# Optimization experiments

Measured on AMD Instinct MI355X. Metric: run time of the kernel, lower is better.

## Reference

```python
import jax, jax.numpy as jnp
import numpy as np

B, C, E, H = 8, 2048, 1024, 128


def setup_inputs() -> dict:
    key = jax.random.key(0)
    k1, k2, k3, k4 = jax.random.split(key, 4)
    x = jax.random.normal(k1, (B, C, E), dtype=jnp.float32)
    # store projection weights as (E, H) so projection is x @ W
    Wq = jax.random.normal(k2, (E, H), dtype=jnp.float32) * (E ** -0.5)
    Wk = jax.random.normal(k3, (E, H), dtype=jnp.float32) * (E ** -0.5)
    Wv = jax.random.normal(k4, (E, H), dtype=jnp.float32) * (E ** -0.5)
    return {"x": x, "Wq": Wq, "Wk": Wk, "Wv": Wv}


def reference(x, Wq, Wk, Wv):
    # x: (B, C, E) -> out: (B, C, H)
    _, c, e = x.shape
    q = x @ Wq  # (B, C, H)
    k = x @ Wk  # (B, C, H)
    v = x @ Wv  # (B, C, H)
    # NOTE: original scales by embed_size**0.5, not head_size**0.5
    scale = jnp.asarray(e, x.dtype) ** 0.5
    w = jnp.einsum('bqh,bkh->bqk', q, k) / scale  # (B, C, C)
    causal = jnp.tril(jnp.ones((c, c), dtype=bool))
    w = jnp.where(causal, w, -jnp.inf)
    w = jax.nn.softmax(w, axis=-1)
    # dropout_rate = 0.0 -> identity (eval mode)
    out = w @ v  # (B, C, H)
    return out
```

## Files before the change

### kernel.cpp

```cpp
#include <hip/hip_runtime.h>
#include <hip/hip_bf16.h>
#include <stdint.h>

#define B_ 8
#define C_ 2048
#define E_ 1024
#define H_ 128
#define M_ (B_*C_)
#define SLOTS_B 144

typedef __attribute__((ext_vector_type(8))) short bf16x8;
typedef __attribute__((ext_vector_type(4))) float f32x4;

__device__ __forceinline__ unsigned short f2bf(float f) {
    union { float f; unsigned int u; } v; v.f = f;
    unsigned int u = v.u;
    u += 0x7fff + ((u >> 16) & 1);
    return (unsigned short)(u >> 16);
}
__device__ __forceinline__ float bf2f(unsigned short u) {
    union { unsigned int i; float f; } v; v.i = ((unsigned int)u) << 16; return v.f;
}

#define GLOAD_LDS16(g, l) \
    __builtin_amdgcn_global_load_lds((const __attribute__((address_space(1))) void*)(g), \
                                     (__attribute__((address_space(3))) void*)(l), 16, 0, 0)

__global__ __launch_bounds__(256) void wt_kernel(const float* __restrict__ Wq,
                                                 const float* __restrict__ Wk,
                                                 const float* __restrict__ Wv,
                                                 unsigned short* __restrict__ WT) {
    int z = blockIdx.y;
    const float* W = (z == 0) ? Wq : (z == 1) ? Wk : Wv;
    unsigned short* o = WT + (size_t)z * H_ * E_;
    int idx = blockIdx.x * 256 + threadIdx.x;
    int e = idx & (E_ - 1), h = idx >> 10;
    o[(size_t)h * E_ + e] = f2bf(W[(size_t)e * H_ + h]);
}

__global__ __launch_bounds__(256) void proj_kernel(const float* __restrict__ x,
                                                   const unsigned short* __restrict__ WT,
                                                   unsigned short* __restrict__ QKV) {
    __shared__ __align__(16) unsigned short As[2][64][64];
    __shared__ __align__(16) unsigned short Bs[2][128][64];

    const int tid = threadIdx.x;
    const int wid = tid >> 6, lane = tid & 63;
    const int lrow = lane & 15, lq = lane >> 4;
    const int wr = wid >> 1, wc = wid & 1;
    const int row0 = blockIdx.x * 64;
    const int w = blockIdx.y;
    const unsigned short* wt = WT + (size_t)w * H_ * E_;

    const int arow = tid >> 2;
    const int ag0 = (tid & 3) * 2;
    const float* xrow = x + (size_t)(row0 + arow) * E_ + ag0 * 8;

    f32x4 acc[2][4];
#pragma unroll
    for (int mi = 0; mi < 2; ++mi)
#pragma unroll
        for (int ni = 0; ni < 4; ++ni) acc[mi][ni] = (f32x4){0.f, 0.f, 0.f, 0.f};

    float4 a0, a1, a2, a3;
    auto A_LOAD = [&](int t) {
        const float* xs = xrow + t * 64;
        a0 = *(const float4*)xs;       a1 = *(const float4*)(xs + 4);
        a2 = *(const float4*)(xs + 8); a3 = *(const float4*)(xs + 12);
    };
    auto A_WRITE = [&](int buf) {
        unsigned short t0[8] = {f2bf(a0.x), f2bf(a0.y), f2bf(a0.z), f2bf(a0.w),
                                f2bf(a1.x), f2bf(a1.y), f2bf(a1.z), f2bf(a1.w)};
        unsigned short t1[8] = {f2bf(a2.x), f2bf(a2.y), f2bf(a2.z), f2bf(a2.w),
                                f2bf(a3.x), f2bf(a3.y), f2bf(a3.z), f2bf(a3.w)};
        *(bf16x8*)&As[buf][arow][(ag0 ^ (arow & 7)) * 8]       = *(const bf16x8*)t0;
        *(bf16x8*)&As[buf][arow][((ag0 + 1) ^ (arow & 7)) * 8] = *(const bf16x8*)t1;
    };
    auto B_STAGE = [&](int buf, int t) {
#pragma unroll
        for (int s = 0; s < 4; ++s) {
            int brow = s * 32 + (tid >> 3);
            int bg = (tid & 7) ^ (brow & 7);
            GLOAD_LDS16(wt + (size_t)brow * E_ + t * 64 + bg * 8,
                        (char*)&Bs[buf][0][0] + s * 4096 + tid * 16);
        }
    };
    auto COMPUTE = [&](int buf) {
#pragma unroll
        for (int ks = 0; ks < 2; ++ks) {
            const int g = ks * 4 + lq;
            bf16x8 af[2], bfr[4];
#pragma unroll
            for (int mi = 0; mi < 2; ++mi) {
                int ra = wr * 32 + mi * 16 + lrow;
                af[mi] = *(const bf16x8*)&As[buf][ra][(g ^ (ra & 7)) * 8];
            }
#pragma unroll
            for (int ni = 0; ni < 4; ++ni) {
                int rb = wc * 64 + ni * 16 + lrow;
                bfr[ni] = *(const bf16x8*)&Bs[buf][rb][(g ^ (rb & 7)) * 8];
            }
#pragma unroll
            for (int mi = 0; mi < 2; ++mi)
#pragma unroll
                for (int ni = 0; ni < 4; ++ni)
                    acc[mi][ni] = __builtin_amdgcn_mfma_f32_16x16x32_bf16(af[mi], bfr[ni], acc[mi][ni], 0, 0, 0);
        }
    };

    A_LOAD(0);
    B_STAGE(0, 0);
    A_WRITE(0);

    for (int t = 0; t < 16; ++t) {
        const int cur = t & 1;
        __syncthreads();
        if (t < 15) {
            A_LOAD(t + 1);
            B_STAGE(cur ^ 1, t + 1);
        }
        COMPUTE(cur);
        if (t < 15) A_WRITE(cur ^ 1);
    }

    if (w < 2) {
        const float qs = (w == 0) ? 0.03125f : 1.0f;
        unsigned short* outp = QKV + (size_t)w * M_ * H_;
#pragma unroll
        for (int mi = 0; mi < 2; ++mi) {
            int r0 = row0 + wr * 32 + mi * 16 + lq * 4;
#pragma unroll
            for (int ni = 0; ni < 4; ++ni) {
                int col = wc * 64 + ni * 16 + lrow;
#pragma unroll
                for (int r = 0; r < 4; ++r)
                    outp[(size_t)(r0 + r) * H_ + col] = f2bf(acc[mi][ni][r] * qs);
            }
        }
    } else {
        unsigned short* vt = QKV + (size_t)2 * M_ * H_;
        int b = row0 / C_;
        int cbase = row0 % C_;
#pragma unroll
        for (int mi = 0; mi < 2; ++mi) {
            int c0 = cbase + wr * 32 + mi * 16 + lq * 4;
#pragma unroll
            for (int ni = 0; ni < 4; ++ni) {
                int h = wc * 64 + ni * 16 + lrow;
                __align__(8) unsigned short p[4] = {f2bf(acc[mi][ni][0]), f2bf(acc[mi][ni][1]),
                                                    f2bf(acc[mi][ni][2]), f2bf(acc[mi][ni][3])};
                *(uint2*)&vt[((size_t)b * H_ + h) * C_ + c0] = *(const uint2*)p;
            }
        }
    }
}

__global__ __launch_bounds__(256) void attn_kernel(const unsigned short* __restrict__ QKV,
                                                   unsigned short* __restrict__ PO,
                                                   float* __restrict__ ML,
                                                   float* __restrict__ out) {
    __shared__ __align__(16) unsigned short Ks[2][64][128];
    __shared__ __align__(16) unsigned short Vt[2][128][64];
    __shared__ __align__(16) unsigned short Ps[4][16][72];

    const unsigned short* Q  = QKV;
    const unsigned short* K  = QKV + (size_t)M_ * H_;
    const unsigned short* VT = QKV + (size_t)2 * M_ * H_;

    const int tid = threadIdx.x, wid = tid >> 6, lane = tid & 63;
    const int lrow = lane & 15, lq = lane >> 4, lk = lq * 8;
    const int rr = blockIdx.x;
    const int b = blockIdx.y;

    int j = 0;
#pragma unroll
    for (int jj = 1; jj < 32; ++jj) {
        int q = jj >> 2, s = jj & 3;
        if (jj + 2 * q * (q - 1) + s * q <= rr) j = jj;
    }
    const int qj = j >> 2, sj = j & 3;
    const int Cj = j + 2 * qj * (qj - 1) + sj * qj;
    const int c = rr - Cj;
    const int nch = qj + 1;
    const int t0 = c * 4;
    const int t1 = min(t0 + 4, j + 1);

    const int q0w = j * 64 + wid * 16;
    const unsigned short* Kb  = K  + (size_t)b * C_ * H_;
    const unsigned short* VTb = VT + (size_t)b * H_ * C_;
    const int qrow0 = q0w + lq * 4;

    const int krow = tid >> 4, kg = tid & 15;
    const int vrow = tid >> 3, vg = tid & 7;

    bf16x8 qf[4];
#pragma unroll
    for (int kf = 0; kf < 4; ++kf)
        qf[kf] = *(const bf16x8*)&Q[((size_t)b * C_ + q0w + lrow) * H_ + kf * 32 + lk];

    f32x4 o[8];
#pragma unroll
    for (int nf = 0; nf < 8; ++nf) o[nf] = (f32x4){0.f, 0.f, 0.f, 0.f};
    float m[4] = {-INFINITY, -INFINITY, -INFINITY, -INFINITY};
    float l[4] = {0.f, 0.f, 0.f, 0.f};

    auto STAGE = [&](int buf, int t) {
        const int kv0 = t * 64;
#pragma unroll
        for (int s = 0; s < 4; ++s) {
            int r = s * 16 + krow;
            GLOAD_LDS16(&Kb[(size_t)(kv0 + r) * H_ + ((kg ^ (r & 15)) * 8)],
                        (char*)&Ks[buf][0][0] + s * 4096 + tid * 16);
        }
#pragma unroll
        for (int s = 0; s < 4; ++s) {
            int h = s * 32 + vrow;
            GLOAD_LDS16(&VTb[(size_t)h * C_ + kv0 + ((vg ^ (h & 7)) * 8)],
                        (char*)&Vt[buf][0][0] + s * 4096 + tid * 16);
        }
    };

    STAGE(0, t0);

    for (int t = t0; t < t1; ++t) {
        const int cur = (t - t0) & 1;
        __syncthreads();
        if (t + 1 < t1) STAGE(cur ^ 1, t + 1);

        const int kv0 = t * 64;
        f32x4 s[4];
#pragma unroll
        for (int nf = 0; nf < 4; ++nf) {
            s[nf] = (f32x4){0.f, 0.f, 0.f, 0.f};
            const int rk = nf * 16 + lrow;
#pragma unroll
            for (int kf = 0; kf < 4; ++kf) {
                bf16x8 kb = *(const bf16x8*)&Ks[cur][rk][((kf * 4 + lq) ^ (rk & 15)) * 8];
                s[nf] = __builtin_amdgcn_mfma_f32_16x16x32_bf16(qf[kf], kb, s[nf], 0, 0, 0);
            }
        }
        bf16x8 vb[8][2];
#pragma unroll
        for (int nf = 0; nf < 8; ++nf) {
            const int h = nf * 16 + lrow;
#pragma unroll
            for (int kf2 = 0; kf2 < 2; ++kf2)
                vb[nf][kf2] = *(const bf16x8*)&Vt[cur][h][((kf2 * 4 + lq) ^ (h & 7)) * 8];
        }

        if (t == j) {
#pragma unroll
            for (int nf = 0; nf < 4; ++nf) {
                int key = kv0 + nf * 16 + lrow;
#pragma unroll
                for (int r = 0; r < 4; ++r)
                    if (key > qrow0 + r) s[nf][r] = -INFINITY;
            }
        }
        float mt[4] = {-INFINITY, -INFINITY, -INFINITY, -INFINITY};
#pragma unroll
        for (int nf = 0; nf < 4; ++nf)
#pragma unroll
            for (int r = 0; r < 4; ++r) mt[r] = fmaxf(mt[r], s[nf][r]);
#pragma unroll
        for (int r = 0; r < 4; ++r)
#pragma unroll
            for (int off = 1; off < 16; off <<= 1)
                mt[r] = fmaxf(mt[r], __shfl_xor(mt[r], off));

        float corr[4];
#pragma unroll
        for (int r = 0; r < 4; ++r) {
            float mn = fmaxf(m[r], mt[r]);
            corr[r] = __expf(m[r] - mn);
            m[r] = mn;
        }
        float ps[4] = {0.f, 0.f, 0.f, 0.f};
#pragma unroll
        for (int nf = 0; nf < 4; ++nf)
#pragma unroll
            for (int r = 0; r < 4; ++r) {
                float p = __expf(s[nf][r] - m[r]);
                ps[r] += p;
                Ps[wid][lq * 4 + r][nf * 16 + lrow] = f2bf(p);
            }
#pragma unroll
        for (int r = 0; r < 4; ++r) {
#pragma unroll
            for (int off = 1; off < 16; off <<= 1) ps[r] += __shfl_xor(ps[r], off);
            l[r] = l[r] * corr[r] + ps[r];
        }
#pragma unroll
        for (int nf = 0; nf < 8; ++nf)
#pragma unroll
            for (int r = 0; r < 4; ++r) o[nf][r] *= corr[r];

        bf16x8 pa[2];
#pragma unroll
        for (int kf2 = 0; kf2 < 2; ++kf2)
            pa[kf2] = *(const bf16x8*)&Ps[wid][lrow][kf2 * 32 + lk];
#pragma unroll
        for (int nf = 0; nf < 8; ++nf)
#pragma unroll
            for (int kf2 = 0; kf2 < 2; ++kf2)
                o[nf] = __builtin_amdgcn_mfma_f32_16x16x32_bf16(pa[kf2], vb[nf][kf2], o[nf], 0, 0, 0);
    }

    if (nch == 1) {
#pragma unroll
        for (int nf = 0; nf < 8; ++nf) {
            int col = nf * 16 + lrow;
#pragma unroll
            for (int r = 0; r < 4; ++r)
                out[((size_t)b * C_ + qrow0 + r) * H_ + col] = o[nf][r] / l[r];
        }
    } else {
        const int slot = b * SLOTS_B + rr;
        unsigned short* po = PO + (size_t)slot * 64 * 128;
        const int rl0 = wid * 16 + lq * 4;
#pragma unroll
        for (int nf = 0; nf < 8; ++nf) {
            int col = nf * 16 + lrow;
#pragma unroll
            for (int r = 0; r < 4; ++r)
                po[(size_t)(rl0 + r) * 128 + col] = f2bf(o[nf][r]);
        }
        if (lrow == 0) {
            float* ml = ML + (size_t)slot * 128;
#pragma unroll
            for (int r = 0; r < 4; ++r) {
                ml[rl0 + r] = m[r];
                ml[64 + rl0 + r] = l[r];
            }
        }
    }
}

__global__ __launch_bounds__(256) void combine_kernel(const unsigned short* __restrict__ PO,
                                                      const float* __restrict__ ML,
                                                      float* __restrict__ out) {
    const int j = blockIdx.x + 4;
    const int b = blockIdx.y;
    const int q = j >> 2, s = j & 3;
    const int Cj = j + 2 * q * (q - 1) + s * q;
    const int nch = q + 1;
    const int base = b * SLOTS_B + Cj;
    const int row = threadIdx.x >> 2;
    const int colg = (threadIdx.x & 3) * 32;

    float mstar = -INFINITY;
    for (int c = 0; c < nch; ++c)
        mstar = fmaxf(mstar, ML[(size_t)(base + c) * 128 + row]);

    float denom = 0.f;
    float acc[32];
#pragma unroll
    for (int i = 0; i < 32; ++i) acc[i] = 0.f;

    for (int c = 0; c < nch; ++c) {
        float mc = ML[(size_t)(base + c) * 128 + row];
        float lc = ML[(size_t)(base + c) * 128 + 64 + row];
        float w = __expf(mc - mstar);
        denom += w * lc;
        const unsigned short* p = PO + (size_t)(base + c) * 64 * 128 + (size_t)row * 128 + colg;
#pragma unroll
        for (int k = 0; k < 4; ++k) {
            bf16x8 v = *(const bf16x8*)&p[k * 8];
#pragma unroll
            for (int e = 0; e < 8; ++e)
                acc[k * 8 + e] += w * bf2f(((unsigned short*)&v)[e]);
        }
    }
    float inv = 1.f / denom;
    float* op = out + ((size_t)b * C_ + j * 64 + row) * H_ + colg;
#pragma unroll
    for (int k = 0; k < 8; ++k) {
        float4 st = {acc[k * 4] * inv, acc[k * 4 + 1] * inv, acc[k * 4 + 2] * inv, acc[k * 4 + 3] * inv};
        *(float4*)&op[k * 4] = st;
    }
}

extern "C" void kernel_launch(void* const* d_in, const int* in_sizes, int n_in,
                              void* d_out, int out_size, void* d_ws, size_t ws_size,
                              hipStream_t stream) {
    const float* x  = (const float*)d_in[0];
    const float* Wq = (const float*)d_in[1];
    const float* Wk = (const float*)d_in[2];
    const float* Wv = (const float*)d_in[3];
    float* out = (float*)d_out;

    unsigned short* WT  = (unsigned short*)d_ws;
    unsigned short* QKV = WT + (size_t)3 * H_ * E_;
    unsigned short* PO  = QKV + (size_t)3 * M_ * H_;
    float*          ML  = (float*)(PO + (size_t)8 * SLOTS_B * 64 * 128);

    wt_kernel<<<dim3(H_ * E_ / 256, 3), 256, 0, stream>>>(Wq, Wk, Wv, WT);
    proj_kernel<<<dim3(M_ / 64, 3), 256, 0, stream>>>(x, WT, QKV);
    attn_kernel<<<dim3(SLOTS_B, B_), 256, 0, stream>>>(QKV, PO, ML, out);
    combine_kernel<<<dim3(28, B_), 256, 0, stream>>>(PO, ML, out);
}
```

Before: 81.43 us.

## Pre-pack weights in MFMA fragment layout and load B directly into registers

The weight conversion kernel now writes bf16 weights grouped in 8-element k-chunks per column, which is the fragment layout the MFMA B operand expects. The projection kernel drops the LDS staging buffer for B and each wave loads its B fragments straight from global memory into a double-buffered register array, with the k-loop fully unrolled. This removes B's LDS traffic and shared memory use, but each wave now reads weights from global/L2 on its own, and the extra registers may lower occupancy.

```diff
diff --git a/kernel.cpp b/kernel.cpp
--- a/kernel.cpp
+++ b/kernel.cpp
@@ -26,23 +26,26 @@
     __builtin_amdgcn_global_load_lds((const __attribute__((address_space(1))) void*)(g), \
                                      (__attribute__((address_space(3))) void*)(l), 16, 0, 0)
 
-__global__ __launch_bounds__(256) void wt_kernel(const float* __restrict__ Wq,
-                                                 const float* __restrict__ Wk,
-                                                 const float* __restrict__ Wv,
-                                                 unsigned short* __restrict__ WT) {
+__global__ __launch_bounds__(256) void wt2_kernel(const float* __restrict__ Wq,
+                                                  const float* __restrict__ Wk,
+                                                  const float* __restrict__ Wv,
+                                                  unsigned short* __restrict__ WT2) {
     int z = blockIdx.y;
     const float* W = (z == 0) ? Wq : (z == 1) ? Wk : Wv;
-    unsigned short* o = WT + (size_t)z * H_ * E_;
-    int idx = blockIdx.x * 256 + threadIdx.x;
-    int e = idx & (E_ - 1), h = idx >> 10;
-    o[(size_t)h * E_ + e] = f2bf(W[(size_t)e * H_ + h]);
+    unsigned short* o = WT2 + (size_t)z * H_ * E_;
+    int gid = blockIdx.x * 256 + threadIdx.x;
+    int g = gid >> 7, h = gid & 127;
+    unsigned short t[8];
+#pragma unroll
+    for (int j = 0; j < 8; ++j)
+        t[j] = f2bf(W[(size_t)(g * 8 + j) * H_ + h]);
+    *(bf16x8*)&o[(size_t)(g * 128 + h) * 8] = *(const bf16x8*)t;
 }
 
 __global__ __launch_bounds__(256) void proj_kernel(const float* __restrict__ x,
-                                                   const unsigned short* __restrict__ WT,
+                                                   const unsigned short* __restrict__ WT2,
                                                    unsigned short* __restrict__ QKV) {
     __shared__ __align__(16) unsigned short As[2][64][64];
-    __shared__ __align__(16) unsigned short Bs[2][128][64];
 
     const int tid = threadIdx.x;
     const int wid = tid >> 6, lane = tid & 63;
@@ -50,7 +53,7 @@
     const int wr = wid >> 1, wc = wid & 1;
     const int row0 = blockIdx.x * 64;
     const int w = blockIdx.y;
-    const unsigned short* wt = WT + (size_t)w * H_ * E_;
+    const unsigned short* wt = WT2 + (size_t)w * H_ * E_;
 
     const int arow = tid >> 2;
     const int ag0 = (tid & 3) * 2;
@@ -63,6 +66,8 @@
         for (int ni = 0; ni < 4; ++ni) acc[mi][ni] = (f32x4){0.f, 0.f, 0.f, 0.f};
 
     float4 a0, a1, a2, a3;
+    bf16x8 breg[2][8];
+
     auto A_LOAD = [&](int t) {
         const float* xs = xrow + t * 64;
         a0 = *(const float4*)xs;       a1 = *(const float4*)(xs + 4);
@@ -76,50 +81,45 @@
         *(bf16x8*)&As[buf][arow][(ag0 ^ (arow & 7)) * 8]       = *(const bf16x8*)t0;
         *(bf16x8*)&As[buf][arow][((ag0 + 1) ^ (arow & 7)) * 8] = *(const bf16x8*)t1;
     };
-    auto B_STAGE = [&](int buf, int t) {
-#pragma unroll
-        for (int s = 0; s < 4; ++s) {
-            int brow = s * 32 + (tid >> 3);
-            int bg = (tid & 7) ^ (brow & 7);
-            GLOAD_LDS16(wt + (size_t)brow * E_ + t * 64 + bg * 8,
-                        (char*)&Bs[buf][0][0] + s * 4096 + tid * 16);
-        }
-    };
-    auto COMPUTE = [&](int buf) {
-#pragma unroll
-        for (int ks = 0; ks < 2; ++ks) {
-            const int g = ks * 4 + lq;
-            bf16x8 af[2], bfr[4];
-#pragma unroll
-            for (int mi = 0; mi < 2; ++mi) {
-                int ra = wr * 32 + mi * 16 + lrow;
-                af[mi] = *(const bf16x8*)&As[buf][ra][(g ^ (ra & 7)) * 8];
-            }
-#pragma unroll
-            for (int ni = 0; ni < 4; ++ni) {
-                int rb = wc * 64 + ni * 16 + lrow;
-                bfr[ni] = *(const bf16x8*)&Bs[buf][rb][(g ^ (rb & 7)) * 8];
-            }
-#pragma unroll
-            for (int mi = 0; mi < 2; ++mi)
-#pragma unroll
-                for (int ni = 0; ni < 4; ++ni)
-                    acc[mi][ni] = __builtin_amdgcn_mfma_f32_16x16x32_bf16(af[mi], bfr[ni], acc[mi][ni], 0, 0, 0);
-        }
-    };
 
     A_LOAD(0);
-    B_STAGE(0, 0);
+#pragma unroll
+    for (int i = 0; i < 8; ++i) {
+        int g = (i >> 2) * 4 + lq;
+        int rb = wc * 64 + (i & 3) * 16 + lrow;
+        breg[0][i] = *(const bf16x8*)&wt[(size_t)(g * 128 + rb) * 8];
+    }
     A_WRITE(0);
 
+#pragma unroll
     for (int t = 0; t < 16; ++t) {
         const int cur = t & 1;
         __syncthreads();
         if (t < 15) {
             A_LOAD(t + 1);
-            B_STAGE(cur ^ 1, t + 1);
-        }
-        COMPUTE(cur);
+#pragma unroll
+            for (int i = 0; i < 8; ++i) {
+                int g = (t + 1) * 8 + (i >> 2) * 4 + lq;
+                int rb = wc * 64 + (i & 3) * 16 + lrow;
+                breg[cur ^ 1][i] = *(const bf16x8*)&wt[(size_t)(g * 128 + rb) * 8];
+            }
+        }
+#pragma unroll
+        for (int ks = 0; ks < 2; ++ks) {
+            const int g = ks * 4 + lq;
+            bf16x8 af[2];
+#pragma unroll
+            for (int mi = 0; mi < 2; ++mi) {
+                int ra = wr * 32 + mi * 16 + lrow;
+                af[mi] = *(const bf16x8*)&As[cur][ra][(g ^ (ra & 7)) * 8];
+            }
+#pragma unroll
+            for (int mi = 0; mi < 2; ++mi)
+#pragma unroll
+                for (int ni = 0; ni < 4; ++ni)
+                    acc[mi][ni] = __builtin_amdgcn_mfma_f32_16x16x32_bf16(
+                        af[mi], breg[cur][ks * 4 + ni], acc[mi][ni], 0, 0, 0);
+        }
         if (t < 15) A_WRITE(cur ^ 1);
     }
 
@@ -389,13 +389,13 @@
     const float* Wv = (const float*)d_in[3];
     float* out = (float*)d_out;
 
-    unsigned short* WT  = (unsigned short*)d_ws;
-    unsigned short* QKV = WT + (size_t)3 * H_ * E_;
+    unsigned short* WT2 = (unsigned short*)d_ws;
+    unsigned short* QKV = WT2 + (size_t)3 * H_ * E_;
     unsigned short* PO  = QKV + (size_t)3 * M_ * H_;
     float*          ML  = (float*)(PO + (size_t)8 * SLOTS_B * 64 * 128);
 
-    wt_kernel<<<dim3(H_ * E_ / 256, 3), 256, 0, stream>>>(Wq, Wk, Wv, WT);
-    proj_kernel<<<dim3(M_ / 64, 3), 256, 0, stream>>>(x, WT, QKV);
+    wt2_kernel<<<dim3(E_ / 8 * H_ / 256, 3), 256, 0, stream>>>(Wq, Wk, Wv, WT2);
+    proj_kernel<<<dim3(M_ / 64, 3), 256, 0, stream>>>(x, WT2, QKV);
     attn_kernel<<<dim3(SLOTS_B, B_), 256, 0, stream>>>(QKV, PO, ML, out);
     combine_kernel<<<dim3(28, B_), 256, 0, stream>>>(PO, ML, out);
 }
```

Result: slower. 84.89 us (+4.2%).
